# Optimization experiments

Measured on AMD Instinct MI355X. Metric: run time of the kernel, lower is better.

## Reference

```python
import jax, jax.numpy as jnp
import numpy as np

B, S, D, H = 2, 2048, 1024, 16
DK = D // H


def setup_inputs() -> dict:
    key = jax.random.key(0)
    ks = jax.random.split(key, 12)
    s = 1.0 / np.sqrt(D)
    inp = {
        "query": jax.random.normal(ks[0], (B, S, D), jnp.float32),
        "key_": jax.random.normal(ks[1], (B, S, D), jnp.float32),
        "value": jax.random.normal(ks[2], (B, S, D), jnp.float32),
        # causal mask, broadcast over heads: [B, 1, S, S]
        "mask": jnp.broadcast_to(jnp.tril(jnp.ones((S, S), bool)), (B, 1, S, S)),
        "W_q": jax.random.uniform(ks[3], (D, D), jnp.float32, -s, s),
        "b_q": jax.random.uniform(ks[4], (D,), jnp.float32, -s, s),
        "W_k": jax.random.uniform(ks[5], (D, D), jnp.float32, -s, s),
        "b_k": jax.random.uniform(ks[6], (D,), jnp.float32, -s, s),
        "W_v": jax.random.uniform(ks[7], (D, D), jnp.float32, -s, s),
        "b_v": jax.random.uniform(ks[8], (D,), jnp.float32, -s, s),
        "W_o": jax.random.uniform(ks[9], (D, D), jnp.float32, -s, s),
        "b_o": jax.random.uniform(ks[10], (D,), jnp.float32, -s, s),
    }
    return inp


def reference(query, key_, value, mask, W_q, b_q, W_k, b_k, W_v, b_v, W_o, b_o):
    b = query.shape[0]
    # linear projections (torch Linear: x @ W.T + b)
    Q = query @ W_q.T + b_q
    K = key_ @ W_k.T + b_k
    V = value @ W_v.T + b_v
    # [b, S, H, dk] -> [b, H, S, dk]
    Q = Q.reshape(b, -1, H, DK).transpose(0, 2, 1, 3)
    K = K.reshape(b, -1, H, DK).transpose(0, 2, 1, 3)
    V = V.reshape(b, -1, H, DK).transpose(0, 2, 1, 3)
    scores = jnp.einsum("bhqd,bhkd->bhqk", Q, K) / jnp.sqrt(jnp.float32(DK))
    scores = jnp.where(mask, scores, -jnp.inf)
    attn = jax.nn.softmax(scores, axis=-1)
    out = jnp.einsum("bhqk,bhkd->bhqd", attn, V)
    out = out.transpose(0, 2, 1, 3).reshape(b, -1, D)
    return out @ W_o.T + b_o
```

## Files before the change

### kernel.cpp

```cpp
#include <hip/hip_runtime.h>
#include <hip/hip_bf16.h>
#include <stdint.h>

#define B_ 2
#define S_ 2048
#define D_ 1024
#define H_ 16
#define DK_ 64

typedef __attribute__((ext_vector_type(4))) float floatx4;
typedef __attribute__((ext_vector_type(8))) short shortx8;
typedef __attribute__((ext_vector_type(4))) short shortx4;
typedef unsigned short ushort_t;

__device__ inline ushort_t f2bf(float f) {
  union { float f; unsigned u; } v; v.f = f;
  unsigned r = v.u + 0x7FFFu + ((v.u >> 16) & 1u);
  return (ushort_t)(r >> 16);
}

__device__ inline unsigned pack2bf(float lo, float hi) {
  return __builtin_amdgcn_perm(__float_as_uint(hi), __float_as_uint(lo), 0x07060302u);
}

__device__ inline shortx4 mk_sx4(unsigned lo, unsigned hi) {
  union { unsigned u[2]; shortx4 s; } v; v.u[0] = lo; v.u[1] = hi; return v.s;
}

__device__ inline float fast_exp2(float x) {
#if __has_builtin(__builtin_amdgcn_exp2f)
  return __builtin_amdgcn_exp2f(x);
#else
  return __expf(0.69314718056f * x);
#endif
}

__device__ inline void gload_lds16(const void* g, void* l) {
  __builtin_amdgcn_global_load_lds(
      (const __attribute__((address_space(1))) unsigned int*)g,
      (__attribute__((address_space(3))) unsigned int*)l, 16, 0, 0);
}

__device__ inline floatx4 mfma16x16x16bf16(shortx4 a, shortx4 b, floatx4 c) {
#if __has_builtin(__builtin_amdgcn_mfma_f32_16x16x16bf16_1k)
  return __builtin_amdgcn_mfma_f32_16x16x16bf16_1k(a, b, c, 0, 0, 0);
#else
  floatx4 d;
  asm("v_mfma_f32_16x16x16_bf16 %0, %1, %2, %3" : "=v"(d) : "v"(a), "v"(b), "v"(c));
  return d;
#endif
}

struct ConvArgs {
  const float* src[7];
  ushort_t* dst[7];
};

__global__ __launch_bounds__(256) void convert_kernel(ConvArgs a) {
  int blk = blockIdx.x;
  int seg, bis;
  if (blk < 3072) { seg = blk >> 10; bis = blk & 1023; }
  else { int bb = blk - 3072; seg = 3 + (bb >> 8); bis = bb & 255; }
  const float4* src = (const float4*)(a.src[seg]) + (size_t)bis * 1024;
  ushort4* dst = (ushort4*)(a.dst[seg]) + (size_t)bis * 1024;
#pragma unroll
  for (int i = 0; i < 4; ++i) {
    int idx = i * 256 + threadIdx.x;
    float4 v = src[idx];
    ushort4 o;
    o.x = f2bf(v.x); o.y = f2bf(v.y); o.z = f2bf(v.z); o.w = f2bf(v.w);
    dst[idx] = o;
  }
}

template <int TM, bool F32OUT>
__device__ inline void gemm_bt_core(const ushort_t* __restrict__ A,
                                    const ushort_t* __restrict__ W,
                                    const float* __restrict__ bias,
                                    float scl,
                                    void* __restrict__ outp,
                                    int m0, int n0, int N, int K) {
  constexpr int LDSU = (TM + 128) * 32;
  constexpr int GA = TM / 16;
  constexpr int GW = (GA + 8) / 4;
  constexpr int MI = TM / 32;
  __shared__ ushort_t smem[2][LDSU];
  const int tid = threadIdx.x;
  const int wave = tid >> 6;
  const int lane = tid & 63;
  const int quad = lane >> 4;
  const int l16 = lane & 15;
  const int wm = (wave >> 1) * (TM / 2);
  const int wn = (wave & 1) * 64;

  floatx4 acc[MI][4] = {};

  const ushort_t* gsrc[GW];
  int ldst[GW];
#pragma unroll
  for (int i = 0; i < GW; ++i) {
    int g = wave * GW + i;
    int row = lane >> 2;
    int col = (lane & 3) * 8;
    if (g < GA) {
      gsrc[i] = A + (size_t)(m0 + g * 16 + row) * K + col;
      ldst[i] = g * 512;
    } else {
      gsrc[i] = W + (size_t)(n0 + (g - GA) * 16 + row) * K + col;
      ldst[i] = TM * 32 + (g - GA) * 512;
    }
  }

#pragma unroll
  for (int i = 0; i < GW; ++i) gload_lds16(gsrc[i], &smem[0][ldst[i]]);

  const int niter = K >> 5;
  for (int j = 0; j < niter; ++j) {
    __syncthreads();
    if (j + 1 < niter) {
      const int ko = (j + 1) * 32;
      ushort_t* bufn = smem[(j + 1) & 1];
#pragma unroll
      for (int i = 0; i < GW; ++i) gload_lds16(gsrc[i] + ko, bufn + ldst[i]);
    }
    const ushort_t* aT = smem[j & 1];
    const ushort_t* bT = smem[j & 1] + TM * 32;
    shortx8 af[MI], bf[4];
#pragma unroll
    for (int mi = 0; mi < MI; ++mi)
      af[mi] = *(const shortx8*)(aT + (wm + mi * 16 + l16) * 32 + quad * 8);
#pragma unroll
    for (int ni = 0; ni < 4; ++ni)
      bf[ni] = *(const shortx8*)(bT + (wn + ni * 16 + l16) * 32 + quad * 8);
#pragma unroll
    for (int mi = 0; mi < MI; ++mi)
#pragma unroll
      for (int ni = 0; ni < 4; ++ni)
        acc[mi][ni] = __builtin_amdgcn_mfma_f32_16x16x32_bf16(af[mi], bf[ni], acc[mi][ni], 0, 0, 0);
  }

#pragma unroll
  for (int ni = 0; ni < 4; ++ni) {
    int n = n0 + wn + ni * 16 + l16;
    float bv = bias[n];
#pragma unroll
    for (int mi = 0; mi < MI; ++mi) {
#pragma unroll
      for (int r = 0; r < 4; ++r) {
        int m = m0 + wm + mi * 16 + quad * 4 + r;
        float v = (acc[mi][ni][r] + bv) * scl;
        if (F32OUT) ((float*)outp)[(size_t)m * N + n] = v;
        else ((ushort_t*)outp)[(size_t)m * N + n] = f2bf(v);
      }
    }
  }
}

struct QkvArgs {
  const ushort_t* A[3];
  const ushort_t* W[3];
  const float* bias[3];
  ushort_t* out[3];
  float scale[3];
};

__global__ __launch_bounds__(256) void gemm_qkv_kernel(QkvArgs a) {
  int z = blockIdx.z;
  int m0 = (blockIdx.x * 4 + (blockIdx.y >> 3)) * 128;
  int n0 = (blockIdx.y & 7) * 128;
  gemm_bt_core<128, false>(a.A[z], a.W[z], a.bias[z], a.scale[z], a.out[z],
                           m0, n0, D_, D_);
}

__global__ __launch_bounds__(256) void gemm_out_kernel(const ushort_t* __restrict__ A,
                                                       const ushort_t* __restrict__ W,
                                                       const float* __restrict__ bias,
                                                       float* __restrict__ out) {
  int m0 = (blockIdx.x * 8 + (blockIdx.y >> 3)) * 64;
  int n0 = (blockIdx.y & 7) * 128;
  gemm_bt_core<64, true>(A, W, bias, 1.0f, out, m0, n0, D_, D_);
}

__global__ __launch_bounds__(256) void vtrans_kernel(const ushort_t* __restrict__ Vp,
                                                     ushort_t* __restrict__ Vt) {
  __shared__ ushort_t t_lds[64 * 66];
  const int t = threadIdx.x;
  const int st = blockIdx.x;
  const int bh = blockIdx.y;
  const int b = bh >> 4;
  const size_t hoff = (size_t)(bh & 15) * 64;
  const int s0 = st * 64;
  {
    int rr = t >> 2, c = (t & 3) * 16;
    const ushort_t* src = Vp + ((size_t)b * S_ + s0 + rr) * D_ + hoff + c;
    uint4 a0 = *(const uint4*)src;
    uint4 a1 = *(const uint4*)(src + 8);
    unsigned* dst = (unsigned*)(t_lds + rr * 66 + c);
    dst[0] = a0.x; dst[1] = a0.y; dst[2] = a0.z; dst[3] = a0.w;
    dst[4] = a1.x; dst[5] = a1.y; dst[6] = a1.z; dst[7] = a1.w;
  }
  __syncthreads();
  {
    int d = t >> 2, cs = (t & 3) * 16;
    ushort_t tmp[16];
#pragma unroll
    for (int i = 0; i < 16; ++i) tmp[i] = t_lds[(cs + i) * 66 + d];
    ushort_t* dst = Vt + ((size_t)bh * 64 + d) * S_ + s0 + cs;
    *(uint4*)(dst) = *(const uint4*)(tmp);
    *(uint4*)(dst + 8) = *(const uint4*)(tmp + 8);
  }
}

__global__ __launch_bounds__(256, 2) void attn_kernel(const ushort_t* __restrict__ Qp,
                                                      const ushort_t* __restrict__ Kp,
                                                      const ushort_t* __restrict__ Vt,
                                                      ushort_t* __restrict__ O) {
  const int qt = 15 - (int)blockIdx.x;
  const int h = blockIdx.y;
  const int b = blockIdx.z;
  const int q0 = qt * 128;
  const int tid = threadIdx.x;
  const int wave = tid >> 6;
  const int lane = tid & 63;
  const int quad = lane >> 4;
  const int l16 = lane & 15;

  __shared__ ushort_t smem[2][8192];

  const size_t hoff = (size_t)h * DK_;

  shortx8 qf[2][2];
#pragma unroll
  for (int grp = 0; grp < 2; ++grp) {
    const ushort_t* qrow = Qp + ((size_t)b * S_ + q0 + wave * 32 + grp * 16 + l16) * D_ + hoff;
#pragma unroll
    for (int ks = 0; ks < 2; ++ks)
      qf[grp][ks] = *(const shortx8*)(qrow + ks * 32 + quad * 8);
  }

  const int r8 = lane >> 3;
  const int jj8 = ((lane & 7) ^ r8) * 8;
  const ushort_t* kb[2];
  const ushort_t* vb[2];
#pragma unroll
  for (int g = 0; g < 2; ++g) {
    int r = wave * 16 + g * 8 + r8;
    kb[g] = Kp + ((size_t)b * S_ + r) * D_ + hoff + jj8;
    vb[g] = Vt + ((size_t)(b * H_ + h) * 64 + r) * S_ + jj8;
  }
  const int ldsrow = (wave * 16) * 64;

  floatx4 oacc[2][4] = {};
  float l_run[2] = {0.f, 0.f};
  const int nj = 2 * qt + 2;
  const int qwave_max = q0 + wave * 32 + 31;

#pragma unroll
  for (int g = 0; g < 2; ++g) {
    gload_lds16(kb[g], &smem[0][ldsrow + g * 512]);
    gload_lds16(vb[g], &smem[0][4096 + ldsrow + g * 512]);
  }

  for (int j = 0; j < nj; ++j) {
    __syncthreads();
    if (j + 1 < nj) {
      ushort_t* bufn = smem[(j + 1) & 1];
      const size_t ko = (size_t)(j + 1) * 64 * D_;
      const int vo = (j + 1) * 64;
#pragma unroll
      for (int g = 0; g < 2; ++g) {
        gload_lds16(kb[g] + ko, bufn + ldsrow + g * 512);
        gload_lds16(vb[g] + vo, bufn + 4096 + ldsrow + g * 512);
      }
    }
    if ((j << 6) > qwave_max) continue;
    const ushort_t* k_lds = smem[j & 1];
    const ushort_t* v_lds = smem[j & 1] + 4096;

    floatx4 sacc[2][4];
#pragma unroll
    for (int kkb = 0; kkb < 4; ++kkb) {
      const ushort_t* krow = k_lds + (kkb * 16 + l16) * 64;
      shortx8 af0 = *(const shortx8*)(krow + (quad ^ (l16 & 7)) * 8);
      shortx8 af1 = *(const shortx8*)(krow + ((4 | quad) ^ (l16 & 7)) * 8);
#pragma unroll
      for (int grp = 0; grp < 2; ++grp) {
        floatx4 acc = {0.f, 0.f, 0.f, 0.f};
        acc = __builtin_amdgcn_mfma_f32_16x16x32_bf16(af0, qf[grp][0], acc, 0, 0, 0);
        acc = __builtin_amdgcn_mfma_f32_16x16x32_bf16(af1, qf[grp][1], acc, 0, 0, 0);
        sacc[grp][kkb] = acc;
      }
    }
#pragma unroll
    for (int grp = 0; grp < 2; ++grp) {
      const int qg = q0 + wave * 32 + grp * 16 + l16;
      if ((j << 6) + 63 > q0 + wave * 32 + grp * 16) {
#pragma unroll
        for (int kkb = 0; kkb < 4; ++kkb)
#pragma unroll
          for (int r = 0; r < 4; ++r)
            if ((j << 6) + kkb * 16 + quad * 4 + r > qg) sacc[grp][kkb][r] = -3.0e38f;
      }
    }

    shortx4 pf[2][4];
#pragma unroll
    for (int grp = 0; grp < 2; ++grp) {
      float psum = 0.f;
#pragma unroll
      for (int kkb = 0; kkb < 4; ++kkb) {
        float p0 = fast_exp2(sacc[grp][kkb][0]);
        float p1 = fast_exp2(sacc[grp][kkb][1]);
        float p2 = fast_exp2(sacc[grp][kkb][2]);
        float p3 = fast_exp2(sacc[grp][kkb][3]);
        psum += (p0 + p1) + (p2 + p3);
        pf[grp][kkb] = mk_sx4(pack2bf(p0, p1), pack2bf(p2, p3));
      }
      l_run[grp] += psum;
    }

#pragma unroll
    for (int kkb = 0; kkb < 4; ++kkb) {
      const int jj = ((2 * kkb + (quad >> 1)) ^ (l16 & 7)) * 8 + (quad & 1) * 4;
#pragma unroll
      for (int db = 0; db < 4; ++db) {
        shortx4 vf = *(const shortx4*)(v_lds + (db * 16 + l16) * 64 + jj);
        oacc[0][db] = mfma16x16x16bf16(vf, pf[0][kkb], oacc[0][db]);
        oacc[1][db] = mfma16x16x16bf16(vf, pf[1][kkb], oacc[1][db]);
      }
    }
  }

  __syncthreads();
  ushort_t* sm = &smem[0][0];
#pragma unroll
  for (int grp = 0; grp < 2; ++grp) {
    float l0 = l_run[grp];
    l0 += __shfl_xor(l0, 16);
    l0 += __shfl_xor(l0, 32);
    float inv_l = 1.0f / l0;
    int row = wave * 32 + grp * 16 + l16;
#pragma unroll
    for (int db = 0; db < 4; ++db) {
#pragma unroll
      for (int rr = 0; rr < 2; ++rr) {
        unsigned pk = pack2bf(oacc[grp][db][rr * 2] * inv_l, oacc[grp][db][rr * 2 + 1] * inv_l);
        *(unsigned*)(sm + row * 72 + db * 16 + quad * 4 + rr * 2) = pk;
      }
    }
  }
  __syncthreads();
  {
    int r = tid >> 1, c = (tid & 1) * 32;
    const ushort_t* src = sm + r * 72 + c;
    ushort_t* dst = O + ((size_t)b * S_ + q0 + r) * D_ + hoff + c;
    uint4 v0 = *(const uint4*)(src);
    uint4 v1 = *(const uint4*)(src + 8);
    uint4 v2 = *(const uint4*)(src + 16);
    uint4 v3 = *(const uint4*)(src + 24);
    *(uint4*)(dst) = v0;
    *(uint4*)(dst + 8) = v1;
    *(uint4*)(dst + 16) = v2;
    *(uint4*)(dst + 24) = v3;
  }
}

extern "C" void kernel_launch(void* const* d_in, const int* in_sizes, int n_in,
                              void* d_out, int out_size, void* d_ws, size_t ws_size,
                              hipStream_t stream) {
  (void)in_sizes; (void)n_in; (void)out_size; (void)ws_size;
  char* ws = (char*)d_ws;
  ushort_t* xq = (ushort_t*)(ws + 0);
  ushort_t* xk = (ushort_t*)(ws + 8388608);
  ushort_t* xv = (ushort_t*)(ws + 16777216);
  ushort_t* wq = (ushort_t*)(ws + 25165824);
  ushort_t* wk = (ushort_t*)(ws + 27262976);
  ushort_t* wv = (ushort_t*)(ws + 29360128);
  ushort_t* wo = (ushort_t*)(ws + 31457280);
  ushort_t* Qp = (ushort_t*)(ws + 33554432);
  ushort_t* Kp = (ushort_t*)(ws + 41943040);
  ushort_t* Vp = (ushort_t*)(ws + 50331648);
  ushort_t* Vt = xk;
  ushort_t* O = xq;

  ConvArgs ca;
  ca.src[0] = (const float*)d_in[0];  ca.dst[0] = xq;
  ca.src[1] = (const float*)d_in[1];  ca.dst[1] = xk;
  ca.src[2] = (const float*)d_in[2];  ca.dst[2] = xv;
  ca.src[3] = (const float*)d_in[4];  ca.dst[3] = wq;
  ca.src[4] = (const float*)d_in[6];  ca.dst[4] = wk;
  ca.src[5] = (const float*)d_in[8];  ca.dst[5] = wv;
  ca.src[6] = (const float*)d_in[10]; ca.dst[6] = wo;
  convert_kernel<<<dim3(4096), dim3(256), 0, stream>>>(ca);

  QkvArgs qa;
  qa.A[0] = xq; qa.W[0] = wq; qa.bias[0] = (const float*)d_in[5]; qa.out[0] = Qp;
  qa.A[1] = xk; qa.W[1] = wk; qa.bias[1] = (const float*)d_in[7]; qa.out[1] = Kp;
  qa.A[2] = xv; qa.W[2] = wv; qa.bias[2] = (const float*)d_in[9]; qa.out[2] = Vp;
  qa.scale[0] = 0.125f * 1.44269504089f;
  qa.scale[1] = 1.0f;
  qa.scale[2] = 1.0f;
  gemm_qkv_kernel<<<dim3(8, 32, 3), dim3(256), 0, stream>>>(qa);

  vtrans_kernel<<<dim3(32, 32), dim3(256), 0, stream>>>(Vp, Vt);

  attn_kernel<<<dim3(16, 16, 2), dim3(256), 0, stream>>>(Qp, Kp, Vt, O);

  gemm_out_kernel<<<dim3(8, 64, 1), dim3(256), 0, stream>>>(
      O, wo, (const float*)d_in[11], (float*)d_out);
}
```

Before: 237.7 us.

## Fuse V transpose into QKV GEMM epilogue and flatten attention grid

The V projection's epilogue now writes its output directly in transposed [b, d, s] layout with packed 32-bit stores, so the separate vtrans kernel and its extra read and write of V are removed. The attention launch becomes a 1D grid where the query-tile order is reversed only for batch 0, interleaving heavy and light causal tiles across the two batches for load balance. The transposed-store epilogue writes strided 8-byte chunks, which coalesce less well than the row-major stores.

```diff
diff --git a/kernel.cpp b/kernel.cpp
--- a/kernel.cpp
+++ b/kernel.cpp
@@ -73,7 +73,7 @@
   }
 }
 
-template <int TM, bool F32OUT>
+template <int TM, int OUTMODE>
 __device__ inline void gemm_bt_core(const ushort_t* __restrict__ A,
                                     const ushort_t* __restrict__ W,
                                     const float* __restrict__ bias,
@@ -145,12 +145,24 @@
     float bv = bias[n];
 #pragma unroll
     for (int mi = 0; mi < MI; ++mi) {
-#pragma unroll
-      for (int r = 0; r < 4; ++r) {
-        int m = m0 + wm + mi * 16 + quad * 4 + r;
-        float v = (acc[mi][ni][r] + bv) * scl;
-        if (F32OUT) ((float*)outp)[(size_t)m * N + n] = v;
-        else ((ushort_t*)outp)[(size_t)m * N + n] = f2bf(v);
+      if (OUTMODE == 2) {
+        int m = m0 + wm + mi * 16 + quad * 4;
+        int b = m >> 11, s = m & 2047;
+        ushort_t* dst = (ushort_t*)outp + (((size_t)(b * 1024 + n)) << 11) + s;
+        unsigned lo = (unsigned)f2bf(acc[mi][ni][0] + bv) |
+                      ((unsigned)f2bf(acc[mi][ni][1] + bv) << 16);
+        unsigned hi = (unsigned)f2bf(acc[mi][ni][2] + bv) |
+                      ((unsigned)f2bf(acc[mi][ni][3] + bv) << 16);
+        *(unsigned*)(dst) = lo;
+        *(unsigned*)(dst + 2) = hi;
+      } else {
+#pragma unroll
+        for (int r = 0; r < 4; ++r) {
+          int m = m0 + wm + mi * 16 + quad * 4 + r;
+          float v = (acc[mi][ni][r] + bv) * scl;
+          if (OUTMODE == 1) ((float*)outp)[(size_t)m * N + n] = v;
+          else ((ushort_t*)outp)[(size_t)m * N + n] = f2bf(v);
+        }
       }
     }
   }
@@ -168,8 +180,10 @@
   int z = blockIdx.z;
   int m0 = (blockIdx.x * 4 + (blockIdx.y >> 3)) * 128;
   int n0 = (blockIdx.y & 7) * 128;
-  gemm_bt_core<128, false>(a.A[z], a.W[z], a.bias[z], a.scale[z], a.out[z],
-                           m0, n0, D_, D_);
+  if (z == 2)
+    gemm_bt_core<128, 2>(a.A[2], a.W[2], a.bias[2], 1.0f, a.out[2], m0, n0, D_, D_);
+  else
+    gemm_bt_core<128, 0>(a.A[z], a.W[z], a.bias[z], a.scale[z], a.out[z], m0, n0, D_, D_);
 }
 
 __global__ __launch_bounds__(256) void gemm_out_kernel(const ushort_t* __restrict__ A,
@@ -178,46 +192,18 @@
                                                        float* __restrict__ out) {
   int m0 = (blockIdx.x * 8 + (blockIdx.y >> 3)) * 64;
   int n0 = (blockIdx.y & 7) * 128;
-  gemm_bt_core<64, true>(A, W, bias, 1.0f, out, m0, n0, D_, D_);
-}
-
-__global__ __launch_bounds__(256) void vtrans_kernel(const ushort_t* __restrict__ Vp,
-                                                     ushort_t* __restrict__ Vt) {
-  __shared__ ushort_t t_lds[64 * 66];
-  const int t = threadIdx.x;
-  const int st = blockIdx.x;
-  const int bh = blockIdx.y;
-  const int b = bh >> 4;
-  const size_t hoff = (size_t)(bh & 15) * 64;
-  const int s0 = st * 64;
-  {
-    int rr = t >> 2, c = (t & 3) * 16;
-    const ushort_t* src = Vp + ((size_t)b * S_ + s0 + rr) * D_ + hoff + c;
-    uint4 a0 = *(const uint4*)src;
-    uint4 a1 = *(const uint4*)(src + 8);
-    unsigned* dst = (unsigned*)(t_lds + rr * 66 + c);
-    dst[0] = a0.x; dst[1] = a0.y; dst[2] = a0.z; dst[3] = a0.w;
-    dst[4] = a1.x; dst[5] = a1.y; dst[6] = a1.z; dst[7] = a1.w;
-  }
-  __syncthreads();
-  {
-    int d = t >> 2, cs = (t & 3) * 16;
-    ushort_t tmp[16];
-#pragma unroll
-    for (int i = 0; i < 16; ++i) tmp[i] = t_lds[(cs + i) * 66 + d];
-    ushort_t* dst = Vt + ((size_t)bh * 64 + d) * S_ + s0 + cs;
-    *(uint4*)(dst) = *(const uint4*)(tmp);
-    *(uint4*)(dst + 8) = *(const uint4*)(tmp + 8);
-  }
+  gemm_bt_core<64, 1>(A, W, bias, 1.0f, out, m0, n0, D_, D_);
 }
 
 __global__ __launch_bounds__(256, 2) void attn_kernel(const ushort_t* __restrict__ Qp,
                                                       const ushort_t* __restrict__ Kp,
                                                       const ushort_t* __restrict__ Vt,
                                                       ushort_t* __restrict__ O) {
-  const int qt = 15 - (int)blockIdx.x;
-  const int h = blockIdx.y;
-  const int b = blockIdx.z;
+  const int id = blockIdx.x;
+  const int h = id & 15;
+  const int qq = (id & 255) >> 4;
+  const int b = id >> 8;
+  const int qt = b ? qq : 15 - qq;
   const int q0 = qt * 128;
   const int tid = threadIdx.x;
   const int wave = tid >> 6;
@@ -379,8 +365,7 @@
   ushort_t* wo = (ushort_t*)(ws + 31457280);
   ushort_t* Qp = (ushort_t*)(ws + 33554432);
   ushort_t* Kp = (ushort_t*)(ws + 41943040);
-  ushort_t* Vp = (ushort_t*)(ws + 50331648);
-  ushort_t* Vt = xk;
+  ushort_t* Vt = (ushort_t*)(ws + 50331648);
   ushort_t* O = xq;
 
   ConvArgs ca;
@@ -396,15 +381,13 @@
   QkvArgs qa;
   qa.A[0] = xq; qa.W[0] = wq; qa.bias[0] = (const float*)d_in[5]; qa.out[0] = Qp;
   qa.A[1] = xk; qa.W[1] = wk; qa.bias[1] = (const float*)d_in[7]; qa.out[1] = Kp;
-  qa.A[2] = xv; qa.W[2] = wv; qa.bias[2] = (const float*)d_in[9]; qa.out[2] = Vp;
+  qa.A[2] = xv; qa.W[2] = wv; qa.bias[2] = (const float*)d_in[9]; qa.out[2] = Vt;
   qa.scale[0] = 0.125f * 1.44269504089f;
   qa.scale[1] = 1.0f;
   qa.scale[2] = 1.0f;
   gemm_qkv_kernel<<<dim3(8, 32, 3), dim3(256), 0, stream>>>(qa);
 
-  vtrans_kernel<<<dim3(32, 32), dim3(256), 0, stream>>>(Vp, Vt);
-
-  attn_kernel<<<dim3(16, 16, 2), dim3(256), 0, stream>>>(Qp, Kp, Vt, O);
+  attn_kernel<<<dim3(512), dim3(256), 0, stream>>>(Qp, Kp, Vt, O);
 
   gemm_out_kernel<<<dim3(8, 64, 1), dim3(256), 0, stream>>>(
       O, wo, (const float*)d_in[11], (float*)d_out);
```

After: 241.2 us. No clear change (+1.5%).
